# Performance work log

Hardware: AMD Instinct MI355X
Metric: run time of the kernel (lower is better)

## Reference

```python
import jax, jax.numpy as jnp
import numpy as np

# Module constants (from init_kwargs)
IN_PLANES = 32
NUM_FILTERS = 4
MAX_H = 128
MAX_W = 128
REPARAM_FACTOR = 8
REPARAM_H = MAX_H * REPARAM_FACTOR  # 1024
REPARAM_W = MAX_W * REPARAM_FACTOR  # 1024
NORMALIZE = True
BATCH = 8


def _init_box_params(key):
    """Random valid boxes (mimics reset_parameters), returned in the
    reparametrized (scaled-down) form stored in the module."""
    k1, k2, k3, k4 = jax.random.split(key, 4)
    shape = (IN_PLANES, NUM_FILTERS)
    # actual box coordinates: x_min < 0 < x_max, comfortably inside the image
    x_min = jax.random.uniform(k1, shape, minval=-MAX_H / 3.0, maxval=-2.0)
    x_max = jax.random.uniform(k2, shape, minval=2.0, maxval=MAX_H / 3.0)
    y_min = jax.random.uniform(k3, shape, minval=-MAX_W / 3.0, maxval=-2.0)
    y_max = jax.random.uniform(k4, shape, minval=2.0, maxval=MAX_W / 3.0)
    # store in reparametrized form (divide by reparametrization scale)
    return (x_min / REPARAM_H, x_max / REPARAM_H,
            y_min / REPARAM_W, y_max / REPARAM_W)


def setup_inputs() -> dict:
    key = jax.random.key(0)
    k_in, k_box = jax.random.split(key)
    inp = jax.random.normal(k_in, (BATCH, IN_PLANES, MAX_H, MAX_W), dtype=jnp.float32)
    x_min, x_max, y_min, y_max = _init_box_params(k_box)
    return {"input": inp,
            "x_min": x_min.astype(jnp.float32), "x_max": x_max.astype(jnp.float32),
            "y_min": y_min.astype(jnp.float32), "y_max": y_max.astype(jnp.float32)}


def reference(input, x_min, x_max, y_min, y_max):
    B, C, H, W = input.shape
    F = x_min.shape[1]

    # undo reparametrization -> actual continuous box coordinates
    xmin = x_min * REPARAM_H
    xmax = x_max * REPARAM_H
    ymin = y_min * REPARAM_W
    ymax = y_max * REPARAM_W

    # integral image with a zero row/col on top/left: ii[b,c,i,j] = sum input[:i,:j]
    ii = jnp.pad(jnp.cumsum(jnp.cumsum(input, axis=2), axis=3),
                 ((0, 0), (0, 0), (1, 0), (1, 0)))  # [B,C,H+1,W+1]

    h_idx = jnp.arange(H, dtype=input.dtype)
    w_idx = jnp.arange(W, dtype=input.dtype)

    # continuous corner coordinates per (channel, filter, output position),
    # clipped into the valid integral-image domain (zero padding outside)
    xs_t = jnp.clip(h_idx[None, None, :] + xmin[:, :, None], 0.0, H)        # [C,F,H]
    xs_b = jnp.clip(h_idx[None, None, :] + xmax[:, :, None] + 1.0, 0.0, H)  # [C,F,H]
    ys_l = jnp.clip(w_idx[None, None, :] + ymin[:, :, None], 0.0, W)        # [C,F,W]
    ys_r = jnp.clip(w_idx[None, None, :] + ymax[:, :, None] + 1.0, 0.0, W)  # [C,F,W]

    c_idx = jnp.arange(C)[:, None, None]  # [C,1,1]

    def x_interp(xs):
        # linear interpolation of integral-image rows at continuous x coords
        x0f = jnp.clip(jnp.floor(xs), 0.0, H - 1.0)   # [C,F,H]
        fx = xs - x0f
        x0 = x0f.astype(jnp.int32)
        r0 = ii[:, c_idx, x0, :]       # [B,C,F,H,W+1]
        r1 = ii[:, c_idx, x0 + 1, :]   # [B,C,F,H,W+1]
        return (1.0 - fx)[None, :, :, :, None] * r0 + fx[None, :, :, :, None] * r1

    def y_interp(rows, ys):
        # linear interpolation along W of x-interpolated integral rows
        y0f = jnp.clip(jnp.floor(ys), 0.0, W - 1.0)   # [C,F,W]
        fy = ys - y0f
        y0 = y0f.astype(jnp.int32)[None, :, :, None, :]  # [1,C,F,1,W]
        tgt = rows.shape[:-1] + (W,)
        g0 = jnp.take_along_axis(rows, jnp.broadcast_to(y0, tgt), axis=-1)
        g1 = jnp.take_along_axis(rows, jnp.broadcast_to(y0 + 1, tgt), axis=-1)
        return (1.0 - fy)[None, :, :, None, :] * g0 + fy[None, :, :, None, :] * g1

    rows_t = x_interp(xs_t)  # top edge
    rows_b = x_interp(xs_b)  # bottom edge

    # inclusion-exclusion over the four bilinearly-sampled corners
    out = (y_interp(rows_b, ys_r) - y_interp(rows_b, ys_l)) \
        - (y_interp(rows_t, ys_r) - y_interp(rows_t, ys_l))   # [B,C,F,H,W]

    if NORMALIZE:
        area = (xmax - xmin + 1.0) * (ymax - ymin + 1.0)  # [C,F]
        out = out / area[None, :, :, None, None]

    return out.reshape(B, C * F, H, W)
```

## Files before the change

### kernel.cpp

```cpp
#include <hip/hip_runtime.h>

#define BATCH 8
#define CC 32
#define FF 4
#define HH 128
#define WW 128
#define STRIDE 129
#define RP 1024.0f

__global__ __launch_bounds__(256) void boxconv_kernel(
    const float* __restrict__ in,
    const float* __restrict__ xmin_p,
    const float* __restrict__ xmax_p,
    const float* __restrict__ ymin_p,
    const float* __restrict__ ymax_p,
    float* __restrict__ out)
{
    __shared__ float ii[(HH + 1) * STRIDE];

    const int plane = blockIdx.x;
    const int c = plane & (CC - 1);
    const int tid = threadIdx.x;
    const float* inp = in + (size_t)plane * (HH * WW);

    for (int i4 = tid; i4 < (HH * WW) / 4; i4 += 256) {
        const float4 v = ((const float4*)inp)[i4];
        const int idx = i4 << 2;
        const int x = idx >> 7;
        const int y = idx & (WW - 1);
        float* dst = &ii[(x + 1) * STRIDE + (y + 1)];
        dst[0] = v.x; dst[1] = v.y; dst[2] = v.z; dst[3] = v.w;
    }
    for (int i = tid; i <= HH; i += 256) {
        ii[i] = 0.0f;
        ii[i * STRIDE] = 0.0f;
    }
    __syncthreads();

    if (tid < HH) {
        float* row = &ii[(tid + 1) * STRIDE + 1];
        float s = 0.0f;
        #pragma unroll 8
        for (int j = 0; j < WW; ++j) { s += row[j]; row[j] = s; }
    }
    __syncthreads();

    if (tid < WW) {
        float* col = &ii[STRIDE + (tid + 1)];
        float s = 0.0f;
        #pragma unroll 8
        for (int x = 0; x < HH; ++x) {
            s += col[x * STRIDE];
            col[x * STRIDE] = s;
        }
    }
    __syncthreads();

    for (int f = 0; f < FF; ++f) {
        const int pidx = c * FF + f;
        const float xmn = xmin_p[pidx] * RP;
        const float xmx = xmax_p[pidx] * RP;
        const float ymn = ymin_p[pidx] * RP;
        const float ymx = ymax_p[pidx] * RP;
        const float inv_area = 1.0f / ((xmx - xmn + 1.0f) * (ymx - ymn + 1.0f));
        float* outp = out + ((size_t)plane * FF + f) * (HH * WW);

        for (int i = tid; i < HH * WW; i += 256) {
            const int h = i >> 7;
            const int w = i & (WW - 1);

            const float xs_t = fminf(fmaxf((float)h + xmn, 0.0f), 128.0f);
            const float x0tf = fminf(floorf(xs_t), 127.0f);
            const float fxt  = xs_t - x0tf;
            const float xs_b = fminf(fmaxf((float)h + xmx + 1.0f, 0.0f), 128.0f);
            const float x0bf = fminf(floorf(xs_b), 127.0f);
            const float fxb  = xs_b - x0bf;

            const float ys_l = fminf(fmaxf((float)w + ymn, 0.0f), 128.0f);
            const float y0lf = fminf(floorf(ys_l), 127.0f);
            const float fyl  = ys_l - y0lf;
            const float ys_r = fminf(fmaxf((float)w + ymx + 1.0f, 0.0f), 128.0f);
            const float y0rf = fminf(floorf(ys_r), 127.0f);
            const float fyr  = ys_r - y0rf;

            const int x0t = (int)x0tf, x0b = (int)x0bf;
            const int y0l = (int)y0lf, y0r = (int)y0rf;

            const float* pt = &ii[x0t * STRIDE];
            const float* pb = &ii[x0b * STRIDE];

            const float rt_l0  = pt[y0l];           const float rt_l1  = pt[y0l + 1];
            const float rt_l0b = pt[y0l + STRIDE];  const float rt_l1b = pt[y0l + 1 + STRIDE];
            const float rt_r0  = pt[y0r];           const float rt_r1  = pt[y0r + 1];
            const float rt_r0b = pt[y0r + STRIDE];  const float rt_r1b = pt[y0r + 1 + STRIDE];
            const float rb_l0  = pb[y0l];           const float rb_l1  = pb[y0l + 1];
            const float rb_l0b = pb[y0l + STRIDE];  const float rb_l1b = pb[y0l + 1 + STRIDE];
            const float rb_r0  = pb[y0r];           const float rb_r1  = pb[y0r + 1];
            const float rb_r0b = pb[y0r + STRIDE];  const float rb_r1b = pb[y0r + 1 + STRIDE];

            const float gxt = 1.0f - fxt, gxb = 1.0f - fxb;
            const float rowt_l0 = gxt * rt_l0 + fxt * rt_l0b;
            const float rowt_l1 = gxt * rt_l1 + fxt * rt_l1b;
            const float rowt_r0 = gxt * rt_r0 + fxt * rt_r0b;
            const float rowt_r1 = gxt * rt_r1 + fxt * rt_r1b;
            const float rowb_l0 = gxb * rb_l0 + fxb * rb_l0b;
            const float rowb_l1 = gxb * rb_l1 + fxb * rb_l1b;
            const float rowb_r0 = gxb * rb_r0 + fxb * rb_r0b;
            const float rowb_r1 = gxb * rb_r1 + fxb * rb_r1b;
            const float T_l = (1.0f - fyl) * rowt_l0 + fyl * rowt_l1;
            const float T_r = (1.0f - fyr) * rowt_r0 + fyr * rowt_r1;
            const float B_l = (1.0f - fyl) * rowb_l0 + fyl * rowb_l1;
            const float B_r = (1.0f - fyr) * rowb_r0 + fyr * rowb_r1;

            outp[i] = ((B_r - B_l) - (T_r - T_l)) * inv_area;
        }
    }
}

extern "C" void kernel_launch(void* const* d_in, const int* in_sizes, int n_in,
                              void* d_out, int out_size, void* d_ws, size_t ws_size,
                              hipStream_t stream) {
    const float* inp    = (const float*)d_in[0];
    const float* x_min  = (const float*)d_in[1];
    const float* x_max  = (const float*)d_in[2];
    const float* y_min  = (const float*)d_in[3];
    const float* y_max  = (const float*)d_in[4];
    float* out = (float*)d_out;

    dim3 grid(BATCH * CC);
    dim3 block(256);
    boxconv_kernel<<<grid, block, 0, stream>>>(inp, x_min, x_max, y_min, y_max, out);
}
```

Measured before the change: 120.3 us.

## Factor x-interpolation into per-row difference buffer and parallelize prefix sums

Each wave now handles one output row. It first builds a per-row difference of the x-interpolated bottom and top integral rows in shared memory, then does only four lookups per output instead of sixteen. Y-interpolation parameters are precomputed once per filter into shared memory. The row and column prefix scans are split into segments across 1024 threads with partial-sum offsets, and block size grows from 256 to 1024. The trade-off is more barriers and extra shared memory in exchange for far fewer LDS reads and serial scan steps.

New measurement: 101.9 us. 1.18x faster.

```diff
diff --git a/kernel.cpp b/kernel.cpp
--- a/kernel.cpp
+++ b/kernel.cpp
@@ -7,8 +7,11 @@
 #define WW 128
 #define STRIDE 129
 #define RP 1024.0f
+#define NTHREADS 1024
+#define NWAVES 16
+#define DSTRIDE 132
 
-__global__ __launch_bounds__(256) void boxconv_kernel(
+__global__ __launch_bounds__(NTHREADS) void boxconv_kernel(
     const float* __restrict__ in,
     const float* __restrict__ xmin_p,
     const float* __restrict__ xmax_p,
@@ -17,13 +20,18 @@
     float* __restrict__ out)
 {
     __shared__ float ii[(HH + 1) * STRIDE];
+    __shared__ float dd[NWAVES * DSTRIDE];
+    __shared__ float partial[8 * 128];
+    __shared__ float4 ypar[WW];
 
     const int plane = blockIdx.x;
     const int c = plane & (CC - 1);
     const int tid = threadIdx.x;
+    const int wave = tid >> 6;
+    const int lane = tid & 63;
     const float* inp = in + (size_t)plane * (HH * WW);
 
-    for (int i4 = tid; i4 < (HH * WW) / 4; i4 += 256) {
+    for (int i4 = tid; i4 < (HH * WW) / 4; i4 += NTHREADS) {
         const float4 v = ((const float4*)inp)[i4];
         const int idx = i4 << 2;
         const int x = idx >> 7;
@@ -31,88 +39,100 @@
         float* dst = &ii[(x + 1) * STRIDE + (y + 1)];
         dst[0] = v.x; dst[1] = v.y; dst[2] = v.z; dst[3] = v.w;
     }
-    for (int i = tid; i <= HH; i += 256) {
-        ii[i] = 0.0f;
-        ii[i * STRIDE] = 0.0f;
+    if (tid <= HH) {
+        ii[tid] = 0.0f;
+        ii[tid * STRIDE] = 0.0f;
     }
     __syncthreads();
 
-    if (tid < HH) {
-        float* row = &ii[(tid + 1) * STRIDE + 1];
+    {
+        const int row = tid & 127, seg = tid >> 7;
+        float* p = &ii[(row + 1) * STRIDE + 1 + seg * 16];
+        float v[16];
         float s = 0.0f;
-        #pragma unroll 8
-        for (int j = 0; j < WW; ++j) { s += row[j]; row[j] = s; }
+        #pragma unroll
+        for (int j = 0; j < 16; ++j) { s += p[j]; v[j] = s; }
+        partial[seg * 128 + row] = s;
+        __syncthreads();
+        float off = 0.0f;
+        for (int k = 0; k < seg; ++k) off += partial[k * 128 + row];
+        #pragma unroll
+        for (int j = 0; j < 16; ++j) p[j] = v[j] + off;
     }
     __syncthreads();
 
-    if (tid < WW) {
-        float* col = &ii[STRIDE + (tid + 1)];
+    {
+        const int col = tid & 127, seg = tid >> 7;
+        float* p = &ii[(seg * 16 + 1) * STRIDE + col + 1];
+        float v[16];
         float s = 0.0f;
-        #pragma unroll 8
-        for (int x = 0; x < HH; ++x) {
-            s += col[x * STRIDE];
-            col[x * STRIDE] = s;
-        }
+        #pragma unroll
+        for (int j = 0; j < 16; ++j) { s += p[j * STRIDE]; v[j] = s; }
+        partial[seg * 128 + col] = s;
+        __syncthreads();
+        float off = 0.0f;
+        for (int k = 0; k < seg; ++k) off += partial[k * 128 + col];
+        #pragma unroll
+        for (int j = 0; j < 16; ++j) p[j * STRIDE] = v[j] + off;
     }
-    __syncthreads();
 
+    float* Dw = &dd[wave * DSTRIDE];
     for (int f = 0; f < FF; ++f) {
         const int pidx = c * FF + f;
+        __syncthreads();
+        if (tid < WW) {
+            const float ymn = ymin_p[pidx] * RP;
+            const float ymx = ymax_p[pidx] * RP;
+            const float w = (float)tid;
+            const float ys_l = fminf(fmaxf(w + ymn, 0.0f), 128.0f);
+            const float y0lf = fminf(floorf(ys_l), 127.0f);
+            const float ys_r = fminf(fmaxf(w + ymx + 1.0f, 0.0f), 128.0f);
+            const float y0rf = fminf(floorf(ys_r), 127.0f);
+            ypar[tid] = make_float4(ys_l - y0lf, ys_r - y0rf,
+                                    __int_as_float(((int)y0lf) << 2),
+                                    __int_as_float(((int)y0rf) << 2));
+        }
+        __syncthreads();
+
         const float xmn = xmin_p[pidx] * RP;
         const float xmx = xmax_p[pidx] * RP;
         const float ymn = ymin_p[pidx] * RP;
         const float ymx = ymax_p[pidx] * RP;
         const float inv_area = 1.0f / ((xmx - xmn + 1.0f) * (ymx - ymn + 1.0f));
-        float* outp = out + ((size_t)plane * FF + f) * (HH * WW);
+        float* outf = out + ((size_t)plane * FF + f) * (HH * WW);
 
-        for (int i = tid; i < HH * WW; i += 256) {
-            const int h = i >> 7;
-            const int w = i & (WW - 1);
-
+        for (int h = wave; h < HH; h += NWAVES) {
             const float xs_t = fminf(fmaxf((float)h + xmn, 0.0f), 128.0f);
             const float x0tf = fminf(floorf(xs_t), 127.0f);
             const float fxt  = xs_t - x0tf;
             const float xs_b = fminf(fmaxf((float)h + xmx + 1.0f, 0.0f), 128.0f);
             const float x0bf = fminf(floorf(xs_b), 127.0f);
             const float fxb  = xs_b - x0bf;
+            const float gxt = 1.0f - fxt, gxb = 1.0f - fxb;
 
-            const float ys_l = fminf(fmaxf((float)w + ymn, 0.0f), 128.0f);
-            const float y0lf = fminf(floorf(ys_l), 127.0f);
-            const float fyl  = ys_l - y0lf;
-            const float ys_r = fminf(fmaxf((float)w + ymx + 1.0f, 0.0f), 128.0f);
-            const float y0rf = fminf(floorf(ys_r), 127.0f);
-            const float fyr  = ys_r - y0rf;
+            const float* pt = &ii[(int)x0tf * STRIDE];
+            const float* pb = &ii[(int)x0bf * STRIDE];
 
-            const int x0t = (int)x0tf, x0b = (int)x0bf;
-            const int y0l = (int)y0lf, y0r = (int)y0rf;
+            for (int y = lane; y < STRIDE; y += 64) {
+                const float t = gxt * pt[y] + fxt * pt[y + STRIDE];
+                const float b = gxb * pb[y] + fxb * pb[y + STRIDE];
+                Dw[y] = b - t;
+            }
 
-            const float* pt = &ii[x0t * STRIDE];
-            const float* pb = &ii[x0b * STRIDE];
-
-            const float rt_l0  = pt[y0l];           const float rt_l1  = pt[y0l + 1];
-            const float rt_l0b = pt[y0l + STRIDE];  const float rt_l1b = pt[y0l + 1 + STRIDE];
-            const float rt_r0  = pt[y0r];           const float rt_r1  = pt[y0r + 1];
-            const float rt_r0b = pt[y0r + STRIDE];  const float rt_r1b = pt[y0r + 1 + STRIDE];
-            const float rb_l0  = pb[y0l];           const float rb_l1  = pb[y0l + 1];
-            const float rb_l0b = pb[y0l + STRIDE];  const float rb_l1b = pb[y0l + 1 + STRIDE];
-            const float rb_r0  = pb[y0r];           const float rb_r1  = pb[y0r + 1];
-            const float rb_r0b = pb[y0r + STRIDE];  const float rb_r1b = pb[y0r + 1 + STRIDE];
-
-            const float gxt = 1.0f - fxt, gxb = 1.0f - fxb;
-            const float rowt_l0 = gxt * rt_l0 + fxt * rt_l0b;
-            const float rowt_l1 = gxt * rt_l1 + fxt * rt_l1b;
-            const float rowt_r0 = gxt * rt_r0 + fxt * rt_r0b;
-            const float rowt_r1 = gxt * rt_r1 + fxt * rt_r1b;
-            const float rowb_l0 = gxb * rb_l0 + fxb * rb_l0b;
-            const float rowb_l1 = gxb * rb_l1 + fxb * rb_l1b;
-            const float rowb_r0 = gxb * rb_r0 + fxb * rb_r0b;
-            const float rowb_r1 = gxb * rb_r1 + fxb * rb_r1b;
-            const float T_l = (1.0f - fyl) * rowt_l0 + fyl * rowt_l1;
-            const float T_r = (1.0f - fyr) * rowt_r0 + fyr * rowt_r1;
-            const float B_l = (1.0f - fyl) * rowb_l0 + fyl * rowb_l1;
-            const float B_r = (1.0f - fyr) * rowb_r0 + fyr * rowb_r1;
-
-            outp[i] = ((B_r - B_l) - (T_r - T_l)) * inv_area;
+            float* outr = outf + h * WW;
+            #pragma unroll
+            for (int k = 0; k < 2; ++k) {
+                const int w = lane + (k << 6);
+                const float4 yp = ypar[w];
+                const char* db = (const char*)Dw;
+                const float d_l0 = *(const float*)(db + __float_as_int(yp.z));
+                const float d_l1 = *(const float*)(db + __float_as_int(yp.z) + 4);
+                const float d_r0 = *(const float*)(db + __float_as_int(yp.w));
+                const float d_r1 = *(const float*)(db + __float_as_int(yp.w) + 4);
+                const float R = (1.0f - yp.y) * d_r0 + yp.y * d_r1;
+                const float L = (1.0f - yp.x) * d_l0 + yp.x * d_l1;
+                outr[w] = (R - L) * inv_area;
+            }
         }
     }
 }
@@ -128,6 +148,6 @@
     float* out = (float*)d_out;
 
     dim3 grid(BATCH * CC);
-    dim3 block(256);
+    dim3 block(NTHREADS);
     boxconv_kernel<<<grid, block, 0, stream>>>(inp, x_min, x_max, y_min, y_max, out);
 }
```
